# Performance work log

Measured on AMD Instinct MI355X. Metric: run time of the kernel, lower is better.

The kernel has to match this reference:

```python
import jax, jax.numpy as jnp
import numpy as np


def setup_inputs() -> dict:
    key = jax.random.key(0)
    kq, kk, kv, ki, ks = jax.random.split(key, 5)
    B, H, S, D, VD, T = 2, 8, 2048, 64, 64, 128
    q = jax.random.normal(kq, (B, H, S, D), dtype=jnp.float32)
    k = jax.random.normal(kk, (B, H, S, D), dtype=jnp.float32)
    v = jax.random.normal(kv, (B, H, S, VD), dtype=jnp.float32)
    topk_indices = jax.random.randint(ki, (B, S, T), 0, S, dtype=jnp.int64)
    topk_scores = jax.random.uniform(ks, (B, S, T), dtype=jnp.float32)
    return {"q": q, "k": k, "v": v, "topk_indices": topk_indices,
            "topk_scores": topk_scores}


def reference(q, k, v, topk_indices, topk_scores):
    # q: (B,H,S,D), k: (B,H,S,D), v: (B,H,S,VD), topk_indices: (B,S,T)
    head_dim = q.shape[-1]
    scale = head_dim ** (-0.5)

    # Gather selected K/V per query directly (no O(S^2) expansion).
    # For each batch b: kb (H,S,D), idx (S,T) -> kb[:, idx, :] (H,S,T,D)
    gather = jax.vmap(lambda xb, ib: xb[:, ib, :])
    k_g = gather(k, topk_indices)  # (B,H,S,T,D)
    v_g = gather(v, topk_indices)  # (B,H,S,T,VD)

    # (B,H,S,T) scores
    attn_scores = jnp.einsum('bhsd,bhstd->bhst', q, k_g) * scale
    attn_weights = jax.nn.softmax(attn_scores, axis=-1)

    # reweight by indexer scores (broadcast over heads), then renormalize
    attn_weights = attn_weights * topk_scores[:, None, :, :]
    attn_weights = attn_weights / (attn_weights.sum(axis=-1, keepdims=True) + 1e-12)

    # (B,H,S,VD)
    output = jnp.einsum('bhst,bhstd->bhsd', attn_weights, v_g)
    return output
```

## Files before the change

kernel.cpp:

```cpp
#include <hip/hip_runtime.h>
#include <math.h>


#define BB 2
#define HH 8
#define SS 2048
#define DD 64
#define VDD 64
#define TT 128
#define SCALE 0.125f
#define NKV (BB * HH * SS * DD)

typedef __fp16 h2 __attribute__((ext_vector_type(2)));
typedef float  f2 __attribute__((ext_vector_type(2)));

__device__ __forceinline__ float bf_lo(unsigned int u) {
    return __uint_as_float(u << 16);
}
__device__ __forceinline__ float bf_hi(unsigned int u) {
    return __uint_as_float(u);
}
__device__ __forceinline__ unsigned short f2bf_rne(float f) {
    unsigned int u = __float_as_uint(f);
    u += 0x7FFFu + ((u >> 16) & 1u);
    return (unsigned short)(u >> 16);
}
__device__ __forceinline__ unsigned int pk_f16(float x, float y) {
    h2 p = __builtin_amdgcn_cvt_pkrtz(x, y);
    return __builtin_bit_cast(unsigned int, p);
}
__device__ __forceinline__ float dot2(unsigned int qh, unsigned int kh, float c) {
    return __builtin_amdgcn_fdot2(__builtin_bit_cast(h2, qh),
                                  __builtin_bit_cast(h2, kh), c, false);
}

__global__ __launch_bounds__(256) void cvt_kv(
    const float* __restrict__ k, const float* __restrict__ v,
    unsigned int* __restrict__ kh, unsigned int* __restrict__ vb)
{
    int i = (blockIdx.x * 256 + threadIdx.x) * 4;
    if (i >= NKV) return;
    float4 kf = *(const float4*)(k + i);
    float4 vf = *(const float4*)(v + i);
    unsigned int k0 = pk_f16(kf.x, kf.y);
    unsigned int k1 = pk_f16(kf.z, kf.w);
    unsigned int v0 = (unsigned int)f2bf_rne(vf.x) | ((unsigned int)f2bf_rne(vf.y) << 16);
    unsigned int v1 = (unsigned int)f2bf_rne(vf.z) | ((unsigned int)f2bf_rne(vf.w) << 16);
    *(uint2*)(kh + i / 2) = make_uint2(k0, k1);
    *(uint2*)(vb + i / 2) = make_uint2(v0, v1);
}

__global__ __launch_bounds__(256, 4) void dsa_sparse_attn_bf16(
    const float* __restrict__ q,
    const unsigned int* __restrict__ kh,
    const unsigned int* __restrict__ vb,
    const int* __restrict__ topk_idx,
    const float* __restrict__ topk_sc,
    float* __restrict__ out)
{
    const int tid  = threadIdx.x;
    const int wave = tid >> 6;
    const int lane = tid & 63;
    const int h    = lane & 7;
    const int g    = lane >> 3;

    const int plane = blockIdx.x & 15;
    const int s     = (blockIdx.x >> 4) * 4 + wave;
    const int b     = plane >> 3;

    const float*        qp  = q  + ((size_t)plane * SS + s) * DD;
    const unsigned int* kp  = kh + (size_t)plane * SS * (DD / 2);
    const unsigned int* vp  = vb + (size_t)plane * SS * (VDD / 2);
    const int*          ip  = topk_idx + ((size_t)b * SS + s) * TT;
    const float*        scp = topk_sc  + ((size_t)b * SS + s) * TT;
    float*              op  = out + ((size_t)plane * SS + s) * VDD;

    int   iv0 = ip[lane];
    int   iv1 = ip[64 + lane];
    float sv0 = scp[lane];
    float sv1 = scp[64 + lane];
    float4 qa = *(const float4*)(qp + h * 8);
    float4 qb = *(const float4*)(qp + h * 8 + 4);
    unsigned int q0 = pk_f16(qa.x * SCALE, qa.y * SCALE);
    unsigned int q1 = pk_f16(qa.z * SCALE, qa.w * SCALE);
    unsigned int q2 = pk_f16(qb.x * SCALE, qb.y * SCALE);
    unsigned int q3 = pk_f16(qb.z * SCALE, qb.w * SCALE);

    float sco[16];
    #pragma unroll
    for (int tc = 0; tc < 8; ++tc) {
        int idx = __shfl(iv0, tc * 8 + g);
        uint4 kk = *(const uint4*)(kp + (size_t)idx * 32 + h * 4);
        float acc = dot2(q0, kk.x, dot2(q1, kk.y, dot2(q2, kk.z, dot2(q3, kk.w, 0.f))));
        acc += __shfl_xor(acc, 1);
        acc += __shfl_xor(acc, 2);
        acc += __shfl_xor(acc, 4);
        sco[tc] = acc;
    }
    #pragma unroll
    for (int tc = 0; tc < 8; ++tc) {
        int idx = __shfl(iv1, tc * 8 + g);
        uint4 kk = *(const uint4*)(kp + (size_t)idx * 32 + h * 4);
        float acc = dot2(q0, kk.x, dot2(q1, kk.y, dot2(q2, kk.z, dot2(q3, kk.w, 0.f))));
        acc += __shfl_xor(acc, 1);
        acc += __shfl_xor(acc, 2);
        acc += __shfl_xor(acc, 4);
        sco[8 + tc] = acc;
    }

    float m = sco[0];
    #pragma unroll
    for (int tc = 1; tc < 16; ++tc) m = fmaxf(m, sco[tc]);
    m = fmaxf(m, __shfl_xor(m, 8));
    m = fmaxf(m, __shfl_xor(m, 16));
    m = fmaxf(m, __shfl_xor(m, 32));

    f2 a0 = {0.f, 0.f}, a1 = {0.f, 0.f}, a2 = {0.f, 0.f}, a3 = {0.f, 0.f};
    float sum = 0.f;
    #pragma unroll
    for (int tc = 0; tc < 8; ++tc) {
        int   idx = __shfl(iv0, tc * 8 + g);
        uint4 u   = *(const uint4*)(vp + (size_t)idx * 32 + h * 4);
        float e   = __expf(sco[tc] - m) * __shfl(sv0, tc * 8 + g);
        sum += e;
        f2 wv = {e, e};
        f2 vx = {bf_lo(u.x), bf_hi(u.x)};
        f2 vy = {bf_lo(u.y), bf_hi(u.y)};
        f2 vz = {bf_lo(u.z), bf_hi(u.z)};
        f2 vw = {bf_lo(u.w), bf_hi(u.w)};
        a0 = __builtin_elementwise_fma(wv, vx, a0);
        a1 = __builtin_elementwise_fma(wv, vy, a1);
        a2 = __builtin_elementwise_fma(wv, vz, a2);
        a3 = __builtin_elementwise_fma(wv, vw, a3);
    }
    #pragma unroll
    for (int tc = 0; tc < 8; ++tc) {
        int   idx = __shfl(iv1, tc * 8 + g);
        uint4 u   = *(const uint4*)(vp + (size_t)idx * 32 + h * 4);
        float e   = __expf(sco[8 + tc] - m) * __shfl(sv1, tc * 8 + g);
        sum += e;
        f2 wv = {e, e};
        f2 vx = {bf_lo(u.x), bf_hi(u.x)};
        f2 vy = {bf_lo(u.y), bf_hi(u.y)};
        f2 vz = {bf_lo(u.z), bf_hi(u.z)};
        f2 vw = {bf_lo(u.w), bf_hi(u.w)};
        a0 = __builtin_elementwise_fma(wv, vx, a0);
        a1 = __builtin_elementwise_fma(wv, vy, a1);
        a2 = __builtin_elementwise_fma(wv, vz, a2);
        a3 = __builtin_elementwise_fma(wv, vw, a3);
    }

    sum += __shfl_xor(sum, 8);
    sum += __shfl_xor(sum, 16);
    sum += __shfl_xor(sum, 32);

    float a[8] = {a0.x, a0.y, a1.x, a1.y, a2.x, a2.y, a3.x, a3.y};
    #pragma unroll
    for (int j = 0; j < 8; ++j) {
        a[j] += __shfl_xor(a[j], 8);
        a[j] += __shfl_xor(a[j], 16);
        a[j] += __shfl_xor(a[j], 32);
    }
    if (g == 0) {
        float inv = 1.0f / (sum + 1e-12f);
        *(float4*)(op + h * 8)     = make_float4(a[0] * inv, a[1] * inv, a[2] * inv, a[3] * inv);
        *(float4*)(op + h * 8 + 4) = make_float4(a[4] * inv, a[5] * inv, a[6] * inv, a[7] * inv);
    }
}

__global__ __launch_bounds__(256, 4) void dsa_sparse_attn_f32(
    const float* __restrict__ q,
    const float* __restrict__ k,
    const float* __restrict__ v,
    const int* __restrict__ topk_idx,
    const float* __restrict__ topk_sc,
    float* __restrict__ out)
{
    const int tid  = threadIdx.x;
    const int wave = tid >> 6;
    const int lane = tid & 63;
    const int plane = blockIdx.x & 15;
    const int s     = (blockIdx.x >> 4) * 4 + wave;
    const int b     = plane >> 3;

    const float* qp  = q + ((size_t)plane * SS + s) * DD;
    const float* kp  = k + (size_t)plane * SS * DD;
    const float* vp  = v + (size_t)plane * SS * VDD;
    const int*   ip  = topk_idx + ((size_t)b * SS + s) * TT;
    const float* scp = topk_sc  + ((size_t)b * SS + s) * TT;
    float*       op  = out + ((size_t)plane * SS + s) * VDD;

    __shared__ int   s_idx[4][TT];
    __shared__ float s_w[4][TT];

    float sc0 = scp[lane];
    float sc1 = scp[64 + lane];
    s_idx[wave][lane]      = ip[lane];
    s_idx[wave][64 + lane] = ip[64 + lane];

    const int l = lane & 3;
    const int g = lane >> 2;
    float4 qf[4];
    #pragma unroll
    for (int j = 0; j < 4; ++j) qf[j] = *(const float4*)(qp + l * 4 + 16 * j);
    __syncthreads();

    #pragma unroll
    for (int tc = 0; tc < 8; ++tc) {
        int t = tc * 16 + g;
        const float* krow = kp + (size_t)s_idx[wave][t] * DD;
        float acc = 0.f;
        #pragma unroll
        for (int j = 0; j < 4; ++j) {
            float4 kf = *(const float4*)(krow + l * 4 + 16 * j);
            acc += qf[j].x * kf.x + qf[j].y * kf.y + qf[j].z * kf.z + qf[j].w * kf.w;
        }
        acc += __shfl_xor(acc, 1);
        acc += __shfl_xor(acc, 2);
        if (l == 0) s_w[wave][t] = acc * SCALE;
    }
    __syncthreads();

    float a0 = s_w[wave][lane];
    float a1 = s_w[wave][64 + lane];
    float m = fmaxf(a0, a1);
    #pragma unroll
    for (int off = 32; off >= 1; off >>= 1) m = fmaxf(m, __shfl_xor(m, off));
    float e0 = __expf(a0 - m) * sc0;
    float e1 = __expf(a1 - m) * sc1;
    float sum = e0 + e1;
    #pragma unroll
    for (int off = 32; off >= 1; off >>= 1) sum += __shfl_xor(sum, off);
    float inv = 1.0f / (sum + 1e-12f);
    s_w[wave][lane]      = e0 * inv;
    s_w[wave][64 + lane] = e1 * inv;
    __syncthreads();

    float acc = 0.f;
    #pragma unroll 8
    for (int t = 0; t < TT; ++t)
        acc = fmaf(s_w[wave][t], vp[(size_t)s_idx[wave][t] * VDD + lane], acc);
    op[lane] = acc;
}

extern "C" void kernel_launch(void* const* d_in, const int* in_sizes, int n_in,
                              void* d_out, int out_size, void* d_ws, size_t ws_size,
                              hipStream_t stream) {
    const float* q   = (const float*)d_in[0];
    const float* k   = (const float*)d_in[1];
    const float* v   = (const float*)d_in[2];
    const int*   idx = (const int*)d_in[3];
    const float* sc  = (const float*)d_in[4];
    float*       out = (float*)d_out;

    const size_t need = (size_t)NKV * 2 * 2;
    if (ws_size >= need) {
        unsigned int* kh = (unsigned int*)d_ws;
        unsigned int* vb = kh + NKV / 2;
        hipLaunchKernelGGL(cvt_kv, dim3(NKV / 4 / 256), dim3(256), 0, stream,
                           k, v, kh, vb);
        hipLaunchKernelGGL(dsa_sparse_attn_bf16, dim3(8192), dim3(256), 0, stream,
                           q, kh, vb, idx, sc, out);
    } else {
        hipLaunchKernelGGL(dsa_sparse_attn_f32, dim3(8192), dim3(256), 0, stream,
                           q, k, v, idx, sc, out);
    }
}
```

Baseline: 125.1 us.

## Fuse QK and PV passes with online softmax and exp2 scaling

Replaces the two-pass score-then-accumulate structure with a single pass using online softmax. K and V rows for each gathered index are loaded together, and the running max, sum and accumulator are rescaled per element. Log2e is folded into the query scale so exp2 can be used. The cross-lane reduction now merges per-lane (max, sum, acc) states. This removes the second index shuffle and the sco array and overlaps the K and V gathers, but it adds two exp2 calls plus rescale FMAs per element and a heavier final reduction.

```diff
diff --git a/kernel.cpp b/kernel.cpp
--- a/kernel.cpp
+++ b/kernel.cpp
@@ -9,6 +9,7 @@
 #define VDD 64
 #define TT 128
 #define SCALE 0.125f
+#define LOG2E 1.44269504088896340736f
 #define NKV (BB * HH * SS * DD)
 
 typedef __fp16 h2 __attribute__((ext_vector_type(2)));
@@ -81,86 +82,84 @@
     float sv1 = scp[64 + lane];
     float4 qa = *(const float4*)(qp + h * 8);
     float4 qb = *(const float4*)(qp + h * 8 + 4);
-    unsigned int q0 = pk_f16(qa.x * SCALE, qa.y * SCALE);
-    unsigned int q1 = pk_f16(qa.z * SCALE, qa.w * SCALE);
-    unsigned int q2 = pk_f16(qb.x * SCALE, qb.y * SCALE);
-    unsigned int q3 = pk_f16(qb.z * SCALE, qb.w * SCALE);
-
-    float sco[16];
-    #pragma unroll
-    for (int tc = 0; tc < 8; ++tc) {
-        int idx = __shfl(iv0, tc * 8 + g);
-        uint4 kk = *(const uint4*)(kp + (size_t)idx * 32 + h * 4);
-        float acc = dot2(q0, kk.x, dot2(q1, kk.y, dot2(q2, kk.z, dot2(q3, kk.w, 0.f))));
-        acc += __shfl_xor(acc, 1);
-        acc += __shfl_xor(acc, 2);
-        acc += __shfl_xor(acc, 4);
-        sco[tc] = acc;
-    }
-    #pragma unroll
-    for (int tc = 0; tc < 8; ++tc) {
-        int idx = __shfl(iv1, tc * 8 + g);
-        uint4 kk = *(const uint4*)(kp + (size_t)idx * 32 + h * 4);
-        float acc = dot2(q0, kk.x, dot2(q1, kk.y, dot2(q2, kk.z, dot2(q3, kk.w, 0.f))));
-        acc += __shfl_xor(acc, 1);
-        acc += __shfl_xor(acc, 2);
-        acc += __shfl_xor(acc, 4);
-        sco[8 + tc] = acc;
-    }
-
-    float m = sco[0];
-    #pragma unroll
-    for (int tc = 1; tc < 16; ++tc) m = fmaxf(m, sco[tc]);
-    m = fmaxf(m, __shfl_xor(m, 8));
-    m = fmaxf(m, __shfl_xor(m, 16));
-    m = fmaxf(m, __shfl_xor(m, 32));
-
+    const float QS = SCALE * LOG2E;
+    unsigned int q0 = pk_f16(qa.x * QS, qa.y * QS);
+    unsigned int q1 = pk_f16(qa.z * QS, qa.w * QS);
+    unsigned int q2 = pk_f16(qb.x * QS, qb.y * QS);
+    unsigned int q3 = pk_f16(qb.z * QS, qb.w * QS);
+
+    float m   = -1e30f;
+    float sum = 0.f;
     f2 a0 = {0.f, 0.f}, a1 = {0.f, 0.f}, a2 = {0.f, 0.f}, a3 = {0.f, 0.f};
-    float sum = 0.f;
+
     #pragma unroll
     for (int tc = 0; tc < 8; ++tc) {
         int   idx = __shfl(iv0, tc * 8 + g);
-        uint4 u   = *(const uint4*)(vp + (size_t)idx * 32 + h * 4);
-        float e   = __expf(sco[tc] - m) * __shfl(sv0, tc * 8 + g);
-        sum += e;
-        f2 wv = {e, e};
-        f2 vx = {bf_lo(u.x), bf_hi(u.x)};
-        f2 vy = {bf_lo(u.y), bf_hi(u.y)};
-        f2 vz = {bf_lo(u.z), bf_hi(u.z)};
-        f2 vw = {bf_lo(u.w), bf_hi(u.w)};
-        a0 = __builtin_elementwise_fma(wv, vx, a0);
-        a1 = __builtin_elementwise_fma(wv, vy, a1);
-        a2 = __builtin_elementwise_fma(wv, vz, a2);
-        a3 = __builtin_elementwise_fma(wv, vw, a3);
+        float sc  = __shfl(sv0, tc * 8 + g);
+        uint4 kk  = *(const uint4*)(kp + (size_t)idx * 32 + h * 4);
+        uint4 vv  = *(const uint4*)(vp + (size_t)idx * 32 + h * 4);
+        float st  = dot2(q0, kk.x, dot2(q1, kk.y, dot2(q2, kk.z, dot2(q3, kk.w, 0.f))));
+        st += __shfl_xor(st, 1);
+        st += __shfl_xor(st, 2);
+        st += __shfl_xor(st, 4);
+        float mn = fmaxf(m, st);
+        float r  = exp2f(m - mn);
+        float e  = exp2f(st - mn) * sc;
+        m = mn;
+        sum = fmaf(sum, r, e);
+        f2 rv = {r, r}, ev = {e, e};
+        f2 vx = {bf_lo(vv.x), bf_hi(vv.x)};
+        f2 vy = {bf_lo(vv.y), bf_hi(vv.y)};
+        f2 vz = {bf_lo(vv.z), bf_hi(vv.z)};
+        f2 vw = {bf_lo(vv.w), bf_hi(vv.w)};
+        a0 = __builtin_elementwise_fma(a0, rv, ev * vx);
+        a1 = __builtin_elementwise_fma(a1, rv, ev * vy);
+        a2 = __builtin_elementwise_fma(a2, rv, ev * vz);
+        a3 = __builtin_elementwise_fma(a3, rv, ev * vw);
     }
     #pragma unroll
     for (int tc = 0; tc < 8; ++tc) {
         int   idx = __shfl(iv1, tc * 8 + g);
-        uint4 u   = *(const uint4*)(vp + (size_t)idx * 32 + h * 4);
-        float e   = __expf(sco[8 + tc] - m) * __shfl(sv1, tc * 8 + g);
-        sum += e;
-        f2 wv = {e, e};
-        f2 vx = {bf_lo(u.x), bf_hi(u.x)};
-        f2 vy = {bf_lo(u.y), bf_hi(u.y)};
-        f2 vz = {bf_lo(u.z), bf_hi(u.z)};
-        f2 vw = {bf_lo(u.w), bf_hi(u.w)};
-        a0 = __builtin_elementwise_fma(wv, vx, a0);
-        a1 = __builtin_elementwise_fma(wv, vy, a1);
-        a2 = __builtin_elementwise_fma(wv, vz, a2);
-        a3 = __builtin_elementwise_fma(wv, vw, a3);
-    }
-
-    sum += __shfl_xor(sum, 8);
-    sum += __shfl_xor(sum, 16);
-    sum += __shfl_xor(sum, 32);
+        float sc  = __shfl(sv1, tc * 8 + g);
+        uint4 kk  = *(const uint4*)(kp + (size_t)idx * 32 + h * 4);
+        uint4 vv  = *(const uint4*)(vp + (size_t)idx * 32 + h * 4);
+        float st  = dot2(q0, kk.x, dot2(q1, kk.y, dot2(q2, kk.z, dot2(q3, kk.w, 0.f))));
+        st += __shfl_xor(st, 1);
+        st += __shfl_xor(st, 2);
+        st += __shfl_xor(st, 4);
+        float mn = fmaxf(m, st);
+        float r  = exp2f(m - mn);
+        float e  = exp2f(st - mn) * sc;
+        m = mn;
+        sum = fmaf(sum, r, e);
+        f2 rv = {r, r}, ev = {e, e};
+        f2 vx = {bf_lo(vv.x), bf_hi(vv.x)};
+        f2 vy = {bf_lo(vv.y), bf_hi(vv.y)};
+        f2 vz = {bf_lo(vv.z), bf_hi(vv.z)};
+        f2 vw = {bf_lo(vv.w), bf_hi(vv.w)};
+        a0 = __builtin_elementwise_fma(a0, rv, ev * vx);
+        a1 = __builtin_elementwise_fma(a1, rv, ev * vy);
+        a2 = __builtin_elementwise_fma(a2, rv, ev * vz);
+        a3 = __builtin_elementwise_fma(a3, rv, ev * vw);
+    }
 
     float a[8] = {a0.x, a0.y, a1.x, a1.y, a2.x, a2.y, a3.x, a3.y};
     #pragma unroll
-    for (int j = 0; j < 8; ++j) {
-        a[j] += __shfl_xor(a[j], 8);
-        a[j] += __shfl_xor(a[j], 16);
-        a[j] += __shfl_xor(a[j], 32);
-    }
+    for (int off = 8; off <= 32; off <<= 1) {
+        float m2 = __shfl_xor(m, off);
+        float s2 = __shfl_xor(sum, off);
+        float mn = fmaxf(m, m2);
+        float r1 = exp2f(m - mn);
+        float r2 = exp2f(m2 - mn);
+        sum = sum * r1 + s2 * r2;
+        #pragma unroll
+        for (int j = 0; j < 8; ++j) {
+            float o = __shfl_xor(a[j], off);
+            a[j] = a[j] * r1 + o * r2;
+        }
+        m = mn;
+    }
+
     if (g == 0) {
         float inv = 1.0f / (sum + 1e-12f);
         *(float4*)(op + h * 8)     = make_float4(a[0] * inv, a[1] * inv, a[2] * inv, a[3] * inv);
```

After: 130.9 us. 1.05x slower.
